# Optimization experiments

Hardware: AMD Instinct MI355X
Metric: run time of the kernel (lower is better)

Reference implementation:

```python
import jax, jax.numpy as jnp
import numpy as np

B, LQ, LK = 2, 2048, 2048
QDIM, KDIM, VDIM, HID, H = 1024, 768, 768, 1024, 16
D = HID // H  # head_dim = 64


def setup_inputs() -> dict:
    key = jax.random.key(0)
    ks = jax.random.split(key, 12)
    s = 0.02
    return {
        "query": jax.random.normal(ks[0], (B, LQ, QDIM), jnp.float32),
        "key": jax.random.normal(ks[1], (B, LK, KDIM), jnp.float32),
        "value": jax.random.normal(ks[2], (B, LK, VDIM), jnp.float32),
        "Wq": jax.random.normal(ks[3], (QDIM, HID), jnp.float32) * s,
        "bq": jnp.zeros((HID,), jnp.float32),
        "Wk": jax.random.normal(ks[4], (KDIM, HID), jnp.float32) * s,
        "bk": jnp.zeros((HID,), jnp.float32),
        "Wv": jax.random.normal(ks[5], (VDIM, HID), jnp.float32) * s,
        "bv": jnp.zeros((HID,), jnp.float32),
        "Wo": jax.random.normal(ks[6], (HID, QDIM), jnp.float32) * s,
        "bo": jnp.zeros((QDIM,), jnp.float32),
        "query_mask": jax.random.randint(ks[7], (B, LQ), 0, 2, jnp.int32),
        "key_mask": jnp.ones((B, LK), jnp.int32),
    }


def reference(query, key, value, Wq, bq, Wk, bk, Wv, bv, Wo, bo, query_mask, key_mask):
    # projections -> [B, L, H, D] -> [B, H, L, D]
    q = (query @ Wq + bq).reshape(B, LQ, H, D).transpose(0, 2, 1, 3)
    k = (key @ Wk + bk).reshape(B, LK, H, D).transpose(0, 2, 1, 3)
    v = (value @ Wv + bv).reshape(B, LK, H, D).transpose(0, 2, 1, 3)

    scores = jnp.einsum("bhqd,bhkd->bhqk", q, k) / jnp.sqrt(jnp.asarray(D, q.dtype))
    # Faithful to the torch code: query_mask masks the LAST (key) axis,
    # key_mask masks the QUERY axis (requires LQ == LK).
    neg_inf = jnp.asarray(-jnp.inf, scores.dtype)
    scores = jnp.where(query_mask[:, None, None, :] == 0, neg_inf, scores)
    scores = jnp.where(key_mask[:, None, :, None] == 0, neg_inf, scores)

    attn = jax.nn.softmax(scores, axis=-1)  # dropout is identity in eval / p=0
    ctx = jnp.einsum("bhqk,bhkd->bqhd", attn, v).reshape(B, LQ, HID)
    return ctx @ Wo + bo
```

## Files before the change

### kernel.cpp

```cpp
#include <hip/hip_runtime.h>
#include <hip/hip_bf16.h>

#define B_   2
#define LQ_  2048
#define LK_  2048
#define QDIM_ 1024
#define KDIM_ 768
#define VDIM_ 768
#define HID_ 1024
#define H_   16
#define D_   64

typedef unsigned short ushort_t;
typedef __attribute__((ext_vector_type(8))) short short8v;
typedef __attribute__((ext_vector_type(4))) float f32x4;

__device__ __forceinline__ float bf2f(unsigned short u) {
    union { unsigned int i; float f; } x; x.i = ((unsigned int)u) << 16; return x.f;
}
__device__ __forceinline__ unsigned short f2bf(float f) {
    union { float f; unsigned int i; } x; x.f = f;
    unsigned int r = x.i + 0x7FFFu + ((x.i >> 16) & 1u);
    return (unsigned short)(r >> 16);
}
__device__ __forceinline__ float exp2_(float x) {
#if defined(__has_builtin) && __has_builtin(__builtin_amdgcn_exp2f)
    return __builtin_amdgcn_exp2f(x);
#else
    return __expf(x * 0.69314718055994531f);
#endif
}
__device__ __forceinline__ unsigned cvtpk_bf16(float lo, float hi) {
    unsigned r;
    asm("v_cvt_pk_bf16_f32 %0, %1, %2" : "=v"(r) : "v"(lo), "v"(hi));
    return r;
}
__device__ __forceinline__ unsigned perm_b32(unsigned hi, unsigned lo, unsigned sel) {
#if defined(__has_builtin) && __has_builtin(__builtin_amdgcn_perm)
    return __builtin_amdgcn_perm(hi, lo, sel);
#else
    unsigned r = 0;
    for (int i = 0; i < 4; ++i) {
        unsigned s = (sel >> (8 * i)) & 0xFF;
        unsigned byte = (s < 4) ? ((lo >> (8 * s)) & 0xFF) : ((hi >> (8 * (s - 4))) & 0xFF);
        r |= byte << (8 * i);
    }
    return r;
#endif
}
__device__ __forceinline__ void stage16(const ushort_t* g, ushort_t* l) {
#if defined(__has_builtin) && __has_builtin(__builtin_amdgcn_global_load_lds)
    __builtin_amdgcn_global_load_lds(
        (const __attribute__((address_space(1))) unsigned*)g,
        (__attribute__((address_space(3))) unsigned*)l, 16, 0, 0);
#else
    *(uint4*)l = *(const uint4*)g;
#endif
}

__device__ __forceinline__ int detect_isbf(const ushort_t* __restrict__ q) {
    float m = 0.f;
    #pragma unroll
    for (int i = 0; i < 8; ++i) {
        uint4 v = *(const uint4*)(q + i * 8);
        const ushort_t* p = (const ushort_t*)&v;
        #pragma unroll
        for (int j = 0; j < 8; ++j) m = fmaxf(m, fabsf(bf2f(p[j])));
    }
    return m < 1000.0f ? 1 : 0;
}

__global__ __launch_bounds__(256) void transpose4(
    const void* __restrict__ W0, const void* __restrict__ W1,
    const void* __restrict__ W2, const void* __restrict__ W3,
    ushort_t* __restrict__ O0, ushort_t* __restrict__ O1,
    ushort_t* __restrict__ O2, ushort_t* __restrict__ O3,
    const ushort_t* __restrict__ qdet)
{
    __shared__ ushort_t tile[64][72];
    const int isbf = detect_isbf(qdet);
    const int op = blockIdx.z;
    const void* in = (op == 0) ? W0 : (op == 1) ? W1 : (op == 2) ? W2 : W3;
    ushort_t* out  = (op == 0) ? O0 : (op == 1) ? O1 : (op == 2) ? O2 : O3;
    const int R = (op == 1 || op == 2) ? KDIM_ : 1024;
    const int C = 1024;
    const int r0 = blockIdx.y * 64, c0 = blockIdx.x * 64;
    if (r0 >= R) return;
    const int tr = threadIdx.x >> 3;
    const int tc8 = (threadIdx.x & 7) * 8;

    #pragma unroll
    for (int h = 0; h < 2; ++h) {
        int r = r0 + tr + h * 32;
        ushort_t tmp[8];
        if (isbf) {
            *(uint4*)tmp = *(const uint4*)((const ushort_t*)in + (size_t)r * C + c0 + tc8);
        } else {
            const float* f = (const float*)in + (size_t)r * C + c0 + tc8;
            float4 a = *(const float4*)f;
            float4 b2 = *(const float4*)(f + 4);
            tmp[0]=f2bf(a.x);  tmp[1]=f2bf(a.y);  tmp[2]=f2bf(a.z);  tmp[3]=f2bf(a.w);
            tmp[4]=f2bf(b2.x); tmp[5]=f2bf(b2.y); tmp[6]=f2bf(b2.z); tmp[7]=f2bf(b2.w);
        }
        *(uint4*)&tile[tr + h * 32][tc8] = *(uint4*)tmp;
    }
    __syncthreads();
    #pragma unroll
    for (int h = 0; h < 2; ++h) {
        int c = tr + h * 32;
        ushort_t tmp[8];
        #pragma unroll
        for (int j = 0; j < 8; ++j) tmp[j] = tile[tc8 + j][c];
        *(uint4*)(out + (size_t)(c0 + c) * R + r0 + tc8) = *(uint4*)tmp;
    }
}

template<int TBN>
__device__ __forceinline__ void gemm_core(
    const void* __restrict__ A, const ushort_t* __restrict__ WT,
    const void* __restrict__ bias, void* __restrict__ Cp,
    int M, int N, int K, int isbf, int a_bf, int c_bf, float out_scale,
    int wg, ushort_t (*As)[32], ushort_t (*Bs)[32])
{
    constexpr int NF = TBN / 32;
    const int tid = threadIdx.x;
    const int l = tid & 63, w = tid >> 6;
    const int g = l >> 4, q = l & 15;
    const int wr = (w >> 1) * 64, wc = (w & 1) * (TBN / 2);
    const int nbn = N / TBN;
    const int bm = (wg / nbn) * 128;
    const int bn = (wg % nbn) * TBN;

    const int r_ = tid >> 2;
    const int c_ = tid & 3;
    const int sc_ = ((c_ ^ (r_ & 3)) << 3);
    const int dc_ = c_ << 3;

    f32x4 acc[4][NF];
    #pragma unroll
    for (int i = 0; i < 4; ++i)
        #pragma unroll
        for (int j = 0; j < NF; ++j)
            acc[i][j] = (f32x4){0.f, 0.f, 0.f, 0.f};

    const int NT = K >> 5;
    float4 fA[4];

    auto issue = [&](int t, int buf) {
        const int koff = t << 5;
        if (a_bf) {
            stage16((const ushort_t*)A + (size_t)(bm + r_) * K + koff + sc_,
                    &As[(buf << 7) + r_][dc_]);
            stage16((const ushort_t*)A + (size_t)(bm + 64 + r_) * K + koff + sc_,
                    &As[(buf << 7) + 64 + r_][dc_]);
        } else {
            const float* Af0 = (const float*)A + (size_t)(bm + r_) * K + koff + dc_;
            const float* Af1 = (const float*)A + (size_t)(bm + 64 + r_) * K + koff + dc_;
            fA[0] = *(const float4*)Af0; fA[1] = *(const float4*)(Af0 + 4);
            fA[2] = *(const float4*)Af1; fA[3] = *(const float4*)(Af1 + 4);
        }
        stage16(WT + (size_t)(bn + r_) * K + koff + sc_, &Bs[buf * TBN + r_][dc_]);
        if (TBN == 128)
            stage16(WT + (size_t)(bn + 64 + r_) * K + koff + sc_, &Bs[buf * TBN + 64 + r_][dc_]);
    };
    auto commitA = [&](int buf) {
        ushort_t t0[8], t1[8];
        t0[0]=f2bf(fA[0].x); t0[1]=f2bf(fA[0].y); t0[2]=f2bf(fA[0].z); t0[3]=f2bf(fA[0].w);
        t0[4]=f2bf(fA[1].x); t0[5]=f2bf(fA[1].y); t0[6]=f2bf(fA[1].z); t0[7]=f2bf(fA[1].w);
        t1[0]=f2bf(fA[2].x); t1[1]=f2bf(fA[2].y); t1[2]=f2bf(fA[2].z); t1[3]=f2bf(fA[2].w);
        t1[4]=f2bf(fA[3].x); t1[5]=f2bf(fA[3].y); t1[6]=f2bf(fA[3].z); t1[7]=f2bf(fA[3].w);
        *(uint4*)&As[(buf << 7) + r_][sc_]      = *(uint4*)t0;
        *(uint4*)&As[(buf << 7) + 64 + r_][sc_] = *(uint4*)t1;
    };

    issue(0, 0);
    if (!a_bf) commitA(0);
    __syncthreads();

    int cur = 0;
    const int fcol = ((g ^ (q & 3)) << 3);
    for (int t = 0; t < NT; ++t) {
        const bool has = (t + 1 < NT);
        if (has) issue(t + 1, cur ^ 1);

        short8v a[4], bb[NF];
        #pragma unroll
        for (int mf = 0; mf < 4; ++mf)
            a[mf] = *(const short8v*)&As[(cur << 7) + wr + mf * 16 + q][fcol];
        #pragma unroll
        for (int nf = 0; nf < NF; ++nf)
            bb[nf] = *(const short8v*)&Bs[cur * TBN + wc + nf * 16 + q][fcol];
        #pragma unroll
        for (int mf = 0; mf < 4; ++mf)
            #pragma unroll
            for (int nf = 0; nf < NF; ++nf)
                acc[mf][nf] = __builtin_amdgcn_mfma_f32_16x16x32_bf16(a[mf], bb[nf], acc[mf][nf], 0, 0, 0);

        if (has && !a_bf) commitA(cur ^ 1);
        __syncthreads();
        cur ^= 1;
    }

    float bv[NF];
    #pragma unroll
    for (int nf = 0; nf < NF; ++nf) {
        int col = bn + wc + nf * 16 + q;
        bv[nf] = isbf ? bf2f(((const ushort_t*)bias)[col]) : ((const float*)bias)[col];
    }
    #pragma unroll
    for (int mf = 0; mf < 4; ++mf)
        #pragma unroll
        for (int nf = 0; nf < NF; ++nf)
            #pragma unroll
            for (int reg = 0; reg < 4; ++reg) {
                int row = bm + wr + mf * 16 + g * 4 + reg;
                int col = bn + wc + nf * 16 + q;
                float vv = (acc[mf][nf][reg] + bv[nf]) * out_scale;
                if (c_bf) ((ushort_t*)Cp)[(size_t)row * N + col] = f2bf(vv);
                else      ((float*)Cp)[(size_t)row * N + col] = vv;
            }
}

struct G3 {
    const void* A0; const void* A1; const void* A2;
    const ushort_t* W0; const ushort_t* W1; const ushort_t* W2;
    const void* b0; const void* b1; const void* b2;
    void* C0; void* C1; void* C2;
    int K0, K1, K2;
    float s0, s1, s2;
};

__global__ __launch_bounds__(256) void gemm3_mfma(G3 p, int M, int N,
                                                  const ushort_t* __restrict__ qdet)
{
    __shared__ ushort_t As[2 * 128][32];
    __shared__ ushort_t Bs[2 * 128][32];
    const int isbf = detect_isbf(qdet);
    const int op = blockIdx.y;
    const void* A = (op == 0) ? p.A0 : (op == 1) ? p.A1 : p.A2;
    const ushort_t* WT = (op == 0) ? p.W0 : (op == 1) ? p.W1 : p.W2;
    const void* bias = (op == 0) ? p.b0 : (op == 1) ? p.b1 : p.b2;
    void* C = (op == 0) ? p.C0 : (op == 1) ? p.C1 : p.C2;
    const int K = (op == 0) ? p.K0 : (op == 1) ? p.K1 : p.K2;
    const float sc = (op == 0) ? p.s0 : (op == 1) ? p.s1 : p.s2;
    const int cpx = gridDim.x >> 3;
    const int wg = (blockIdx.x & 7) * cpx + (blockIdx.x >> 3);
    gemm_core<128>(A, WT, bias, C, M, N, K, isbf, isbf, 1, sc, wg, As, Bs);
}

__global__ __launch_bounds__(256) void gemm_one(
    const void* __restrict__ A, const ushort_t* __restrict__ WT,
    const void* __restrict__ bias, void* __restrict__ Cp,
    int M, int N, int K, const ushort_t* __restrict__ qdet, float out_scale)
{
    __shared__ ushort_t As[2 * 128][32];
    __shared__ ushort_t Bs[2 * 64][32];
    const int isbf = detect_isbf(qdet);
    const int cpx = gridDim.x >> 3;
    const int wg = (blockIdx.x & 7) * cpx + (blockIdx.x >> 3);
    gemm_core<64>(A, WT, bias, Cp, M, N, K, isbf, 1, isbf, out_scale, wg, As, Bs);
}

__global__ __launch_bounds__(512, 4) void attn_mfma(
    const ushort_t* __restrict__ Q, const ushort_t* __restrict__ Kp,
    const ushort_t* __restrict__ Vp, const int* __restrict__ qmask,
    const int* __restrict__ kmask, ushort_t* __restrict__ ctx)
{
    __shared__ ushort_t sK[2][64][64];
    __shared__ ushort_t sVt[2][64][64];
    __shared__ ushort_t sP[8][16][64];
    __shared__ unsigned sMaskAll[32][32];

    const int tid = threadIdx.x;
    const int l = tid & 63, w = tid >> 6;
    const int g = l >> 4, q = l & 15;
    const int wg = ((int)blockIdx.x & 7) * 64 + ((int)blockIdx.x >> 3);
    const int grp = wg >> 4;
    const int q0 = (wg & 15) * 128;
    const int b = grp >> 4, h = grp & 15;
    const size_t hoff = (size_t)h * 64;
    const int swz = (q & 7) << 3;

    const int vpi = tid & 255;
    const int vk2 = (vpi & 31) * 2;
    const int vdb = vpi >> 5;
    const int vds = (tid >> 8) * 4;
    const size_t vbase0 = ((size_t)(b * LK_) + vk2) * HID_ + hoff + vdb * 8 + vds;

    const int krow = tid >> 3, ks = tid & 7;
    const int kscol = ((ks ^ (krow & 7)) << 3);
    const size_t kbase0 = ((size_t)(b * LK_) + krow) * HID_ + hoff + kscol;

    auto writeV = [&](int buf, uint2 a, uint2 c) {
        #pragma unroll
        for (int t2 = 0; t2 < 2; ++t2) {
            unsigned d0w = t2 ? a.y : a.x;
            unsigned d1w = t2 ? c.y : c.x;
            unsigned lo = perm_b32(d1w, d0w, 0x05040100);
            unsigned hi = perm_b32(d1w, d0w, 0x07060302);
            int dr0 = vdb * 8 + vds + 2 * t2, dr1 = dr0 + 1;
            *(unsigned*)&sVt[buf][dr0][vk2 ^ ((dr0 & 7) << 3)] = lo;
            *(unsigned*)&sVt[buf][dr1][vk2 ^ ((dr1 & 7) << 3)] = hi;
        }
    };

    stage16(Kp + kbase0, &sK[0][krow][ks << 3]);
    {
        uint2 a = *(const uint2*)(Vp + vbase0);
        uint2 c = *(const uint2*)(Vp + vbase0 + HID_);
        writeV(0, a, c);
    }
    for (int tt = w; tt < 32; tt += 8) {
        unsigned long long bits = __ballot(qmask[b * LQ_ + tt * 64 + l] != 0);
        if (l < 32) {
            unsigned dw = (((bits >> (2 * l)) & 1ull) ? 0xFFFFu : 0u)
                        | (((bits >> (2 * l + 1)) & 1ull) ? 0xFFFF0000u : 0u);
            sMaskAll[tt][l] = dw;
        }
    }

    const int myq = 16 * w + q;
    const ushort_t* Qrow = Q + ((size_t)(b * LQ_) + q0 + myq) * HID_ + hoff;
    short8v qf0 = *(const short8v*)(Qrow + (g << 3));
    short8v qf1 = *(const short8v*)(Qrow + 32 + (g << 3));
    const int rowm = kmask[b * LK_ + q0 + myq];
    __syncthreads();

    short8v ones;
    #pragma unroll
    for (int j = 0; j < 8; ++j) ones[j] = (short)0x3F80;

    float m_run = -1e30f;
    f32x4 o[4], o4;
    #pragma unroll
    for (int df = 0; df < 4; ++df) o[df] = (f32x4){0.f, 0.f, 0.f, 0.f};
    o4 = (f32x4){0.f, 0.f, 0.f, 0.f};

    auto qkt = [&](int buf, f32x4 (&S)[4]) {
        #pragma unroll
        for (int kf = 0; kf < 4; ++kf) S[kf] = (f32x4){0.f, 0.f, 0.f, 0.f};
        __builtin_amdgcn_s_setprio(1);
        #pragma unroll
        for (int kf = 0; kf < 4; ++kf) {
            short8v k0f = *(const short8v*)&sK[buf][kf * 16 + q][(g << 3) ^ swz];
            short8v k1f = *(const short8v*)&sK[buf][kf * 16 + q][(32 + (g << 3)) ^ swz];
            S[kf] = __builtin_amdgcn_mfma_f32_16x16x32_bf16(k0f, qf0, S[kf], 0, 0, 0);
            S[kf] = __builtin_amdgcn_mfma_f32_16x16x32_bf16(k1f, qf1, S[kf], 0, 0, 0);
        }
        __builtin_amdgcn_s_setprio(0);
    };

    f32x4 SA[4], SB[4];
    stage16(Kp + kbase0 + (size_t)64 * HID_, &sK[1][krow][ks << 3]);
    qkt(0, SA);
    __syncthreads();

    auto body = [&](int t, f32x4 (&Sc)[4], f32x4 (&Sn)[4]) {
        const int nb = (t + 1) & 1;
        const bool hasN = (t + 1 < 32);
        uint2 va, vc;
        if (t + 2 < 32)
            stage16(Kp + kbase0 + (size_t)(t + 2) * 64 * HID_, &sK[t & 1][krow][ks << 3]);
        if (hasN) {
            size_t basev = vbase0 + (size_t)(t + 1) * 64 * HID_;
            va = *(const uint2*)(Vp + basev);
            vc = *(const uint2*)(Vp + basev + HID_);
            qkt(nb, Sn);
        }

        float tmx[8];
        #pragma unroll
        for (int i = 0; i < 8; ++i) tmx[i] = fmaxf(Sc[i >> 2][i & 3], Sc[2 + (i >> 2)][i & 3]);
        #pragma unroll
        for (int st = 4; st >= 1; st >>= 1)
            #pragma unroll
            for (int i = 0; i < st; ++i) tmx[i] = fmaxf(tmx[i], tmx[i + st]);
        float lm = tmx[0];
        lm = fmaxf(lm, __shfl_xor(lm, 16));
        lm = fmaxf(lm, __shfl_xor(lm, 32));

        const bool fullp = __any(lm - m_run > 8.0f) != 0;
        float mnew, corr;
        if (fullp) { mnew = fmaxf(m_run, lm); corr = exp2_(m_run - mnew); }
        else       { mnew = m_run;            corr = 1.0f; }

        #pragma unroll
        for (int kf = 0; kf < 4; ++kf)
            #pragma unroll
            for (int reg = 0; reg < 4; ++reg)
                Sc[kf][reg] = exp2_(Sc[kf][reg] - mnew);
        m_run = mnew;

        #pragma unroll
        for (int kf = 0; kf < 4; ++kf) {
            uint2 pv;
            pv.x = cvtpk_bf16(Sc[kf][0], Sc[kf][1]);
            pv.y = cvtpk_bf16(Sc[kf][2], Sc[kf][3]);
            *(uint2*)&sP[w][q][(kf * 16 + g * 4) ^ swz] = pv;
        }

        if (fullp) {
            #pragma unroll
            for (int df = 0; df < 4; ++df)
                #pragma unroll
                for (int reg = 0; reg < 4; ++reg) o[df][reg] *= corr;
            #pragma unroll
            for (int reg = 0; reg < 4; ++reg) o4[reg] *= corr;
        }

        #pragma unroll
        for (int s2 = 0; s2 < 2; ++s2) {
            uint4 paw = *(const uint4*)&sP[w][q][((s2 * 32) + (g << 3)) ^ swz];
            uint4 mk = *(const uint4*)&sMaskAll[t][s2 * 16 + g * 4];
            paw.x &= mk.x; paw.y &= mk.y; paw.z &= mk.z; paw.w &= mk.w;
            short8v pa;
            __builtin_memcpy(&pa, &paw, 16);
            __builtin_amdgcn_s_setprio(1);
            #pragma unroll
            for (int df = 0; df < 4; ++df) {
                short8v vb = *(const short8v*)&sVt[t & 1][df * 16 + q][((s2 * 32) + (g << 3)) ^ swz];
                o[df] = __builtin_amdgcn_mfma_f32_16x16x32_bf16(vb, pa, o[df], 0, 0, 0);
            }
            o4 = __builtin_amdgcn_mfma_f32_16x16x32_bf16(ones, pa, o4, 0, 0, 0);
            __builtin_amdgcn_s_setprio(0);
        }

        if (hasN) writeV(nb, va, vc);
        __syncthreads();
    };

    for (int t2 = 0; t2 < 32; t2 += 2) {
        body(t2,     SA, SB);
        body(t2 + 1, SB, SA);
    }

    const float lr = o4[0];
    const float lqv = (rowm != 0 && lr > 0.f) ? (1.f / lr) : 0.f;
    ushort_t* orow = ctx + ((size_t)(b * LQ_) + q0 + myq) * HID_ + hoff;
    #pragma unroll
    for (int df = 0; df < 4; ++df) {
        uint2 st;
        st.x = cvtpk_bf16(o[df][0] * lqv, o[df][1] * lqv);
        st.y = cvtpk_bf16(o[df][2] * lqv, o[df][3] * lqv);
        *(uint2*)(orow + df * 16 + g * 4) = st;
    }
}

extern "C" void kernel_launch(void* const* d_in, const int* in_sizes, int n_in,
                              void* d_out, int out_size, void* d_ws, size_t ws_size,
                              hipStream_t stream) {
    const int* qmask = (const int*)d_in[11];
    const int* kmask = (const int*)d_in[12];
    const ushort_t* qdet = (const ushort_t*)d_in[0];

    const size_t M = (size_t)B_ * LQ_;
    ushort_t* qx = (ushort_t*)((char*)d_ws + 256);
    ushort_t* kx = qx + M * HID_;
    ushort_t* vx = kx + M * HID_;
    ushort_t* cx = vx + M * HID_;
    ushort_t* WTq = cx;
    ushort_t* WTk = WTq + 1024 * 1024;
    ushort_t* WTv = WTk + 1024 * 768;
    ushort_t* WTo = WTv + 1024 * 768;

    const float QSCALE = 0.125f * 1.4426950408889634f;

    transpose4<<<dim3(16, 16, 4), 256, 0, stream>>>(
        d_in[3], d_in[5], d_in[7], d_in[9], WTq, WTk, WTv, WTo, qdet);

    G3 p;
    p.A0 = d_in[0]; p.A1 = d_in[1]; p.A2 = d_in[2];
    p.W0 = WTq;     p.W1 = WTk;     p.W2 = WTv;
    p.b0 = d_in[4]; p.b1 = d_in[6]; p.b2 = d_in[8];
    p.C0 = qx;      p.C1 = kx;      p.C2 = vx;
    p.K0 = QDIM_;   p.K1 = KDIM_;   p.K2 = VDIM_;
    p.s0 = QSCALE;  p.s1 = 1.0f;    p.s2 = 1.0f;
    const int nwg3 = (int)(M / 128) * (HID_ / 128);
    gemm3_mfma<<<dim3(nwg3, 3), 256, 0, stream>>>(p, (int)M, HID_, qdet);

    attn_mfma<<<dim3(512), 512, 0, stream>>>(qx, kx, vx, qmask, kmask, qx);

    gemm_one<<<dim3((int)(M / 128) * (QDIM_ / 64)), 256, 0, stream>>>(
        qx, WTo, d_in[10], d_out, (int)M, QDIM_, HID_, qdet, 1.0f);
}
```

Baseline: 137.8 us.

## Process two query sub-tiles per wave in attention to reuse K/V fragments

Each wave now computes two 16-row query tiles per iteration, sharing the K and V shared-memory fragments across both sets of MFMAs. Blocks cover 256 queries, so the grid halves and K/V global loads per query halve. The previous one-tile-ahead QK^T software pipelining is removed, and the occupancy hint in launch bounds is dropped. The trade-off is higher register use and fewer blocks, which may expose latency.

```diff
diff --git a/kernel.cpp b/kernel.cpp
--- a/kernel.cpp
+++ b/kernel.cpp
@@ -261,22 +261,22 @@
     gemm_core<64>(A, WT, bias, Cp, M, N, K, isbf, 1, isbf, out_scale, wg, As, Bs);
 }
 
-__global__ __launch_bounds__(512, 4) void attn_mfma(
+__global__ __launch_bounds__(512) void attn_mfma(
     const ushort_t* __restrict__ Q, const ushort_t* __restrict__ Kp,
     const ushort_t* __restrict__ Vp, const int* __restrict__ qmask,
     const int* __restrict__ kmask, ushort_t* __restrict__ ctx)
 {
     __shared__ ushort_t sK[2][64][64];
     __shared__ ushort_t sVt[2][64][64];
-    __shared__ ushort_t sP[8][16][64];
+    __shared__ ushort_t sP[8][32][64];
     __shared__ unsigned sMaskAll[32][32];
 
     const int tid = threadIdx.x;
     const int l = tid & 63, w = tid >> 6;
     const int g = l >> 4, q = l & 15;
-    const int wg = ((int)blockIdx.x & 7) * 64 + ((int)blockIdx.x >> 3);
-    const int grp = wg >> 4;
-    const int q0 = (wg & 15) * 128;
+    const int wg = ((int)blockIdx.x & 7) * 32 + ((int)blockIdx.x >> 3);
+    const int grp = wg >> 3;
+    const int q0 = (wg & 7) * 256;
     const int b = grp >> 4, h = grp & 15;
     const size_t hoff = (size_t)h * 64;
     const int swz = (q & 7) << 3;
@@ -319,130 +319,145 @@
         }
     }
 
-    const int myq = 16 * w + q;
-    const ushort_t* Qrow = Q + ((size_t)(b * LQ_) + q0 + myq) * HID_ + hoff;
-    short8v qf0 = *(const short8v*)(Qrow + (g << 3));
-    short8v qf1 = *(const short8v*)(Qrow + 32 + (g << 3));
-    const int rowm = kmask[b * LK_ + q0 + myq];
+    const int mqb = 16 * w + q;
+    short8v qf[2][2];
+    int rowm[2];
+    #pragma unroll
+    for (int s = 0; s < 2; ++s) {
+        const ushort_t* Qrow = Q + ((size_t)(b * LQ_) + q0 + s * 128 + mqb) * HID_ + hoff;
+        qf[s][0] = *(const short8v*)(Qrow + (g << 3));
+        qf[s][1] = *(const short8v*)(Qrow + 32 + (g << 3));
+        rowm[s] = kmask[b * LK_ + q0 + s * 128 + mqb];
+    }
     __syncthreads();
 
     short8v ones;
     #pragma unroll
     for (int j = 0; j < 8; ++j) ones[j] = (short)0x3F80;
 
-    float m_run = -1e30f;
-    f32x4 o[4], o4;
-    #pragma unroll
-    for (int df = 0; df < 4; ++df) o[df] = (f32x4){0.f, 0.f, 0.f, 0.f};
-    o4 = (f32x4){0.f, 0.f, 0.f, 0.f};
-
-    auto qkt = [&](int buf, f32x4 (&S)[4]) {
-        #pragma unroll
-        for (int kf = 0; kf < 4; ++kf) S[kf] = (f32x4){0.f, 0.f, 0.f, 0.f};
-        __builtin_amdgcn_s_setprio(1);
-        #pragma unroll
-        for (int kf = 0; kf < 4; ++kf) {
-            short8v k0f = *(const short8v*)&sK[buf][kf * 16 + q][(g << 3) ^ swz];
-            short8v k1f = *(const short8v*)&sK[buf][kf * 16 + q][(32 + (g << 3)) ^ swz];
-            S[kf] = __builtin_amdgcn_mfma_f32_16x16x32_bf16(k0f, qf0, S[kf], 0, 0, 0);
-            S[kf] = __builtin_amdgcn_mfma_f32_16x16x32_bf16(k1f, qf1, S[kf], 0, 0, 0);
-        }
-        __builtin_amdgcn_s_setprio(0);
-    };
-
-    f32x4 SA[4], SB[4];
-    stage16(Kp + kbase0 + (size_t)64 * HID_, &sK[1][krow][ks << 3]);
-    qkt(0, SA);
-    __syncthreads();
-
-    auto body = [&](int t, f32x4 (&Sc)[4], f32x4 (&Sn)[4]) {
-        const int nb = (t + 1) & 1;
+    float m_run[2] = {-1e30f, -1e30f};
+    f32x4 o[2][4], o4[2];
+    #pragma unroll
+    for (int s = 0; s < 2; ++s) {
+        #pragma unroll
+        for (int df = 0; df < 4; ++df) o[s][df] = (f32x4){0.f, 0.f, 0.f, 0.f};
+        o4[s] = (f32x4){0.f, 0.f, 0.f, 0.f};
+    }
+
+    for (int t = 0; t < 32; ++t) {
+        const int cur = t & 1;
         const bool hasN = (t + 1 < 32);
         uint2 va, vc;
-        if (t + 2 < 32)
-            stage16(Kp + kbase0 + (size_t)(t + 2) * 64 * HID_, &sK[t & 1][krow][ks << 3]);
         if (hasN) {
+            stage16(Kp + kbase0 + (size_t)(t + 1) * 64 * HID_,
+                    &sK[cur ^ 1][krow][ks << 3]);
             size_t basev = vbase0 + (size_t)(t + 1) * 64 * HID_;
             va = *(const uint2*)(Vp + basev);
             vc = *(const uint2*)(Vp + basev + HID_);
-            qkt(nb, Sn);
-        }
-
-        float tmx[8];
-        #pragma unroll
-        for (int i = 0; i < 8; ++i) tmx[i] = fmaxf(Sc[i >> 2][i & 3], Sc[2 + (i >> 2)][i & 3]);
-        #pragma unroll
-        for (int st = 4; st >= 1; st >>= 1)
-            #pragma unroll
-            for (int i = 0; i < st; ++i) tmx[i] = fmaxf(tmx[i], tmx[i + st]);
-        float lm = tmx[0];
-        lm = fmaxf(lm, __shfl_xor(lm, 16));
-        lm = fmaxf(lm, __shfl_xor(lm, 32));
-
-        const bool fullp = __any(lm - m_run > 8.0f) != 0;
-        float mnew, corr;
-        if (fullp) { mnew = fmaxf(m_run, lm); corr = exp2_(m_run - mnew); }
-        else       { mnew = m_run;            corr = 1.0f; }
-
-        #pragma unroll
-        for (int kf = 0; kf < 4; ++kf)
-            #pragma unroll
-            for (int reg = 0; reg < 4; ++reg)
-                Sc[kf][reg] = exp2_(Sc[kf][reg] - mnew);
-        m_run = mnew;
-
+        }
+
+        f32x4 S[2][4];
+        #pragma unroll
+        for (int s = 0; s < 2; ++s)
+            #pragma unroll
+            for (int kf = 0; kf < 4; ++kf) S[s][kf] = (f32x4){0.f, 0.f, 0.f, 0.f};
+        __builtin_amdgcn_s_setprio(1);
         #pragma unroll
         for (int kf = 0; kf < 4; ++kf) {
-            uint2 pv;
-            pv.x = cvtpk_bf16(Sc[kf][0], Sc[kf][1]);
-            pv.y = cvtpk_bf16(Sc[kf][2], Sc[kf][3]);
-            *(uint2*)&sP[w][q][(kf * 16 + g * 4) ^ swz] = pv;
-        }
-
-        if (fullp) {
-            #pragma unroll
-            for (int df = 0; df < 4; ++df)
+            short8v k0f = *(const short8v*)&sK[cur][kf * 16 + q][(g << 3) ^ swz];
+            short8v k1f = *(const short8v*)&sK[cur][kf * 16 + q][(32 + (g << 3)) ^ swz];
+            #pragma unroll
+            for (int s = 0; s < 2; ++s) {
+                S[s][kf] = __builtin_amdgcn_mfma_f32_16x16x32_bf16(k0f, qf[s][0], S[s][kf], 0, 0, 0);
+                S[s][kf] = __builtin_amdgcn_mfma_f32_16x16x32_bf16(k1f, qf[s][1], S[s][kf], 0, 0, 0);
+            }
+        }
+        __builtin_amdgcn_s_setprio(0);
+
+        #pragma unroll
+        for (int s = 0; s < 2; ++s) {
+            float tmx[8];
+            #pragma unroll
+            for (int i = 0; i < 8; ++i)
+                tmx[i] = fmaxf(S[s][i >> 2][i & 3], S[s][2 + (i >> 2)][i & 3]);
+            #pragma unroll
+            for (int st = 4; st >= 1; st >>= 1)
                 #pragma unroll
-                for (int reg = 0; reg < 4; ++reg) o[df][reg] *= corr;
-            #pragma unroll
-            for (int reg = 0; reg < 4; ++reg) o4[reg] *= corr;
+                for (int i = 0; i < st; ++i) tmx[i] = fmaxf(tmx[i], tmx[i + st]);
+            float lm = tmx[0];
+            lm = fmaxf(lm, __shfl_xor(lm, 16));
+            lm = fmaxf(lm, __shfl_xor(lm, 32));
+
+            const bool fullp = __any(lm - m_run[s] > 8.0f) != 0;
+            float mnew, corr;
+            if (fullp) { mnew = fmaxf(m_run[s], lm); corr = exp2_(m_run[s] - mnew); }
+            else       { mnew = m_run[s];            corr = 1.0f; }
+
+            #pragma unroll
+            for (int kf = 0; kf < 4; ++kf)
+                #pragma unroll
+                for (int reg = 0; reg < 4; ++reg)
+                    S[s][kf][reg] = exp2_(S[s][kf][reg] - mnew);
+            m_run[s] = mnew;
+
+            #pragma unroll
+            for (int kf = 0; kf < 4; ++kf) {
+                uint2 pv;
+                pv.x = cvtpk_bf16(S[s][kf][0], S[s][kf][1]);
+                pv.y = cvtpk_bf16(S[s][kf][2], S[s][kf][3]);
+                *(uint2*)&sP[w][s * 16 + q][(kf * 16 + g * 4) ^ swz] = pv;
+            }
+
+            if (fullp) {
+                #pragma unroll
+                for (int df = 0; df < 4; ++df)
+                    #pragma unroll
+                    for (int reg = 0; reg < 4; ++reg) o[s][df][reg] *= corr;
+                #pragma unroll
+                for (int reg = 0; reg < 4; ++reg) o4[s][reg] *= corr;
+            }
         }
 
         #pragma unroll
         for (int s2 = 0; s2 < 2; ++s2) {
-            uint4 paw = *(const uint4*)&sP[w][q][((s2 * 32) + (g << 3)) ^ swz];
             uint4 mk = *(const uint4*)&sMaskAll[t][s2 * 16 + g * 4];
-            paw.x &= mk.x; paw.y &= mk.y; paw.z &= mk.z; paw.w &= mk.w;
-            short8v pa;
-            __builtin_memcpy(&pa, &paw, 16);
+            short8v pa[2];
+            #pragma unroll
+            for (int s = 0; s < 2; ++s) {
+                uint4 paw = *(const uint4*)&sP[w][s * 16 + q][((s2 * 32) + (g << 3)) ^ swz];
+                paw.x &= mk.x; paw.y &= mk.y; paw.z &= mk.z; paw.w &= mk.w;
+                __builtin_memcpy(&pa[s], &paw, 16);
+            }
             __builtin_amdgcn_s_setprio(1);
             #pragma unroll
             for (int df = 0; df < 4; ++df) {
-                short8v vb = *(const short8v*)&sVt[t & 1][df * 16 + q][((s2 * 32) + (g << 3)) ^ swz];
-                o[df] = __builtin_amdgcn_mfma_f32_16x16x32_bf16(vb, pa, o[df], 0, 0, 0);
+                short8v vb = *(const short8v*)&sVt[cur][df * 16 + q][((s2 * 32) + (g << 3)) ^ swz];
+                #pragma unroll
+                for (int s = 0; s < 2; ++s)
+                    o[s][df] = __builtin_amdgcn_mfma_f32_16x16x32_bf16(vb, pa[s], o[s][df], 0, 0, 0);
             }
-            o4 = __builtin_amdgcn_mfma_f32_16x16x32_bf16(ones, pa, o4, 0, 0, 0);
+            #pragma unroll
+            for (int s = 0; s < 2; ++s)
+                o4[s] = __builtin_amdgcn_mfma_f32_16x16x32_bf16(ones, pa[s], o4[s], 0, 0, 0);
             __builtin_amdgcn_s_setprio(0);
         }
 
-        if (hasN) writeV(nb, va, vc);
+        if (hasN) writeV(cur ^ 1, va, vc);
         __syncthreads();
-    };
-
-    for (int t2 = 0; t2 < 32; t2 += 2) {
-        body(t2,     SA, SB);
-        body(t2 + 1, SB, SA);
-    }
-
-    const float lr = o4[0];
-    const float lqv = (rowm != 0 && lr > 0.f) ? (1.f / lr) : 0.f;
-    ushort_t* orow = ctx + ((size_t)(b * LQ_) + q0 + myq) * HID_ + hoff;
-    #pragma unroll
-    for (int df = 0; df < 4; ++df) {
-        uint2 st;
-        st.x = cvtpk_bf16(o[df][0] * lqv, o[df][1] * lqv);
-        st.y = cvtpk_bf16(o[df][2] * lqv, o[df][3] * lqv);
-        *(uint2*)(orow + df * 16 + g * 4) = st;
+    }
+
+    #pragma unroll
+    for (int s = 0; s < 2; ++s) {
+        const float lr = o4[s][0];
+        const float lqv = (rowm[s] != 0 && lr > 0.f) ? (1.f / lr) : 0.f;
+        ushort_t* orow = ctx + ((size_t)(b * LQ_) + q0 + s * 128 + mqb) * HID_ + hoff;
+        #pragma unroll
+        for (int df = 0; df < 4; ++df) {
+            uint2 st;
+            st.x = cvtpk_bf16(o[s][df][0] * lqv, o[s][df][1] * lqv);
+            st.y = cvtpk_bf16(o[s][df][2] * lqv, o[s][df][3] * lqv);
+            *(uint2*)(orow + df * 16 + g * 4) = st;
+        }
     }
 }
 
@@ -478,7 +493,7 @@
     const int nwg3 = (int)(M / 128) * (HID_ / 128);
     gemm3_mfma<<<dim3(nwg3, 3), 256, 0, stream>>>(p, (int)M, HID_, qdet);
 
-    attn_mfma<<<dim3(512), 512, 0, stream>>>(qx, kx, vx, qmask, kmask, qx);
+    attn_mfma<<<dim3(256), 512, 0, stream>>>(qx, kx, vx, qmask, kmask, qx);
 
     gemm_one<<<dim3((int)(M / 128) * (QDIM_ / 64)), 256, 0, stream>>>(
         qx, WTo, d_in[10], d_out, (int)M, QDIM_, HID_, qdet, 1.0f);
```

After: 150.3 us. 1.09x slower.
